# Kernel optimization log

Hardware: AMD Instinct MI355X
Metric: run time of the kernel (lower is better)

Reference implementation:

```python
import jax, jax.numpy as jnp
import numpy as np

B, N, D, H, C, TOPK = 1, 1024, 1024, 16, 64, 2
HD = D // H   # head_dim = 64
G = N // C    # num blocks = 16


def setup_inputs() -> dict:
    key = jax.random.key(0)
    ks = jax.random.split(key, 6)
    s = 0.02  # init_std
    x = jax.random.normal(ks[0], (B, N, D), jnp.float32)
    Wq = jax.random.normal(ks[1], (D, D), jnp.float32) * s
    Wk = jax.random.normal(ks[2], (D, D), jnp.float32) * s
    Wv = jax.random.normal(ks[3], (D, D), jnp.float32) * s
    Wg = jax.random.normal(ks[4], (2 * H, D), jnp.float32) * s
    Wo = jax.random.normal(ks[5], (D, D), jnp.float32) * s
    return {"x": x, "Wq": Wq, "Wk": Wk, "Wv": Wv, "Wg": Wg, "Wo": Wo}


def reference(x, Wq, Wk, Wv, Wg, Wo):
    b, n, d = x.shape
    h, c, hd, g = H, C, HD, G
    scale = hd ** -0.5
    # projections (torch Linear: x @ W.T)
    q = (x @ Wq.T).reshape(b, n, h, hd)
    k = (x @ Wk.T).reshape(b, n, h, hd)
    v = (x @ Wv.T).reshape(b, n, h, hd)
    gate = jax.nn.softmax((x @ Wg.T).reshape(b, n, h, 2), axis=-1)
    # chunked views: (b, g, c, h, hd)
    kc = k.reshape(b, g, c, h, hd)
    vc = v.reshape(b, g, c, h, hd)
    # compressed block keys: mean over chunk dim -> (b, g, h, hd)
    k_compress = kc.mean(axis=2)
    # block selection scores (b, h, n, g)
    score = jnp.einsum('bnhd,bghd->bhng', q, k_compress)
    pos = jnp.arange(n)[:, None]
    blk = jnp.arange(g)[None, :]
    mask = pos >= c * blk  # (n, g), exactly as source's _get_mask (masked_fill where True)
    score = jnp.where(mask[None, None], -jnp.inf, score)
    idx = jax.lax.top_k(score, TOPK)[1]  # (b, h, n, top_k), int indices
    # gather selected blocks per (batch, head, query)
    k_bhgcd = kc.transpose(0, 3, 1, 2, 4)  # (b, h, g, c, hd)
    v_bhgcd = vc.transpose(0, 3, 1, 2, 4)
    gather = jax.vmap(jax.vmap(lambda kv, i: kv[i]))  # over b, h
    k_sel = gather(k_bhgcd, idx).reshape(b, h, n, TOPK * c, hd)
    v_sel = gather(v_bhgcd, idx).reshape(b, h, n, TOPK * c, hd)
    # inter: per-query attention over gathered KV (non-causal), flash-attn scale 1/sqrt(hd)
    logits = jnp.einsum('bnhd,bhnld->bhnl', q, k_sel) * scale
    p = jax.nn.softmax(logits, axis=-1)
    o_inter = jnp.einsum('bhnl,bhnld->bnhd', p, v_sel)
    # intra: causal attention within each chunk
    qc = q.reshape(b, g, c, h, hd)
    intra = jnp.einsum('bgihd,bgjhd->bghij', qc, kc) * scale
    cm = jnp.tril(jnp.ones((c, c), dtype=bool))
    intra = jnp.where(cm, intra, -jnp.inf)
    pi = jax.nn.softmax(intra, axis=-1)
    o_intra = jnp.einsum('bghij,bgjhd->bgihd', pi, vc).reshape(b, n, h, hd)
    # gated blend + output projection
    o = gate[..., 0:1] * o_inter + gate[..., 1:2] * o_intra  # (b, n, h, hd)
    return o.reshape(b, n, h * hd) @ Wo.T
```

## Files before the change

kernel.cpp:

```cpp
#include <hip/hip_runtime.h>
#include <hip/hip_bf16.h>
#include <math.h>


typedef __attribute__((ext_vector_type(8))) short short8;
typedef __attribute__((ext_vector_type(4))) float f32x4;

#define NTOK 1024
#define DMODEL 1024
#define NHEAD 16
#define HDIM 64
#define CHUNK 64
#define NBLK 16

__device__ __forceinline__ float qmax16(float v)
{
    #pragma unroll
    for (int off = 1; off < 16; off <<= 1) v = fmaxf(v, __shfl_xor(v, off));
    return v;
}

__device__ __forceinline__ float qsum16(float v)
{
    #pragma unroll
    for (int off = 1; off < 16; off <<= 1) v += __shfl_xor(v, off);
    return v;
}

__global__ __launch_bounds__(256) void prep_kernel(
    const float* __restrict__ x,  const float* __restrict__ Wq,
    const float* __restrict__ Wk, const float* __restrict__ Wv,
    const float* __restrict__ Wo, const float* __restrict__ Wg,
    __hip_bfloat16* __restrict__ xh,  __hip_bfloat16* __restrict__ xl,
    __hip_bfloat16* __restrict__ Wqh,
    __hip_bfloat16* __restrict__ Wkh, __hip_bfloat16* __restrict__ Wvh,
    __hip_bfloat16* __restrict__ Woh, __hip_bfloat16* __restrict__ Wol,
    float* __restrict__ xm, float2* __restrict__ gate)
{
    __shared__ float gs[32];
    const int bid = blockIdx.x;
    if (bid < 5120) {
        const int which = bid >> 10;
        const int b = bid & 1023;
        const int i = (b * 256 + threadIdx.x) * 4;
        const float* in; __hip_bfloat16 *hi, *lo = nullptr;
        if (which == 0)      { in = x;  hi = xh;  lo = xl; }
        else if (which == 1) { in = Wq; hi = Wqh; }
        else if (which == 2) { in = Wk; hi = Wkh; }
        else if (which == 3) { in = Wv; hi = Wvh; }
        else                 { in = Wo; hi = Woh; lo = Wol; }
        float4 v = *(const float4*)(in + i);
        float vv[4] = {v.x, v.y, v.z, v.w};
        __hip_bfloat16 h[4], l[4];
        #pragma unroll
        for (int j = 0; j < 4; j++) {
            h[j] = __float2bfloat16(vv[j]);
            l[j] = __float2bfloat16(vv[j] - __bfloat162float(h[j]));
        }
        *(uint2*)(hi + i) = *(uint2*)h;
        if (lo) *(uint2*)(lo + i) = *(uint2*)l;
    } else if (bid < 5184) {
        const int b = bid - 5120;
        const int g = b >> 2;
        const int f = (b & 3) * 256 + threadIdx.x;
        float s = 0.f;
        #pragma unroll 8
        for (int c = 0; c < CHUNK; c++) s += x[(size_t)(g * CHUNK + c) * DMODEL + f];
        xm[g * DMODEL + f] = s * (1.0f / CHUNK);
    } else {
        const int n = bid - 5184;
        const int wave = threadIdx.x >> 6, lane = threadIdx.x & 63;
        #pragma unroll
        for (int jj = 0; jj < 8; jj++) {
            int j = wave * 8 + jj;
            float s = 0.f;
            #pragma unroll
            for (int t = 0; t < 16; t++) {
                int d = lane + (t << 6);
                s += x[n * DMODEL + d] * Wg[j * DMODEL + d];
            }
            #pragma unroll
            for (int off = 32; off; off >>= 1) s += __shfl_xor(s, off);
            if (lane == 0) gs[j] = s;
        }
        __syncthreads();
        if (threadIdx.x < NHEAD) {
            int h = threadIdx.x;
            float a = gs[2 * h], b = gs[2 * h + 1];
            float m = fmaxf(a, b);
            float ea = expf(a - m), eb = expf(b - m);
            float inv = 1.f / (ea + eb);
            gate[n * NHEAD + h] = make_float2(ea * inv, eb * inv);
        }
    }
}

__global__ __launch_bounds__(256) void kc_gemm_kernel(
    const float* __restrict__ xm, const float* __restrict__ Wk,
    float* __restrict__ kc)
{
    const int f = blockIdx.x;
    const int g = threadIdx.x >> 4;
    const int sub = threadIdx.x & 15;
    const float* wrow = Wk + (size_t)f * DMODEL;
    float s = 0.f;
    #pragma unroll 16
    for (int i = 0; i < 64; i++) {
        int e = i * 16 + sub;
        s += xm[g * DMODEL + e] * wrow[e];
    }
    #pragma unroll
    for (int off = 8; off; off >>= 1) s += __shfl_xor(s, off);
    if (sub == 0) kc[g * DMODEL + f] = s;
}

__global__ __launch_bounds__(256) void u_kernel(
    const float* __restrict__ kc, const float* __restrict__ Wq,
    __hip_bfloat16* __restrict__ Uh, __hip_bfloat16* __restrict__ Ul)
{
    __shared__ float kcs[64];
    const int h = blockIdx.x >> 4, g = blockIdx.x & 15;
    if (threadIdx.x < 64) kcs[threadIdx.x] = kc[g * DMODEL + h * HDIM + threadIdx.x];
    __syncthreads();
    const int col = (h << 4) | g;
    for (int f = threadIdx.x; f < DMODEL; f += 256) {
        float s = 0.f;
        #pragma unroll 16
        for (int d = 0; d < 64; d++)
            s += kcs[d] * Wq[(size_t)(h * HDIM + d) * DMODEL + f];
        __hip_bfloat16 hv = __float2bfloat16(s);
        Uh[(size_t)col * DMODEL + f] = hv;
        Ul[(size_t)col * DMODEL + f] = __float2bfloat16(s - __bfloat162float(hv));
    }
}

__global__ __launch_bounds__(256) void qkv_score_kernel(
    const __hip_bfloat16* __restrict__ xh, const __hip_bfloat16* __restrict__ xl,
    const __hip_bfloat16* __restrict__ Wqh, const __hip_bfloat16* __restrict__ Wkh,
    const __hip_bfloat16* __restrict__ Wvh,
    const __hip_bfloat16* __restrict__ Uh, const __hip_bfloat16* __restrict__ Ul,
    __hip_bfloat16* __restrict__ Qb, __hip_bfloat16* __restrict__ Kb,
    __hip_bfloat16* __restrict__ Vt, float* __restrict__ S)
{
    __shared__ uint4 smem4[36864 / 16];
    char* smem = (char*)smem4;
    const int b = blockIdx.x;

    const int tid  = threadIdx.x;
    const int wave = tid >> 6;
    const int lane = tid & 63;
    const int lr = tid >> 2;
    const int lc = (tid & 3) * 16;
    const int wm = (wave >> 1) * 32;
    const int wn = (wave & 1) * 32;
    const int fr = lane & 15;
    const int quad = lane >> 4;

    if (b < 768) {
        __hip_bfloat16 (*Ash)[72] = (__hip_bfloat16(*)[72])smem;
        __hip_bfloat16 (*Bsh)[72] = (__hip_bfloat16(*)[72])(smem + 9216);

        const int widx = b >> 8;
        const int t = b & 255;
        const __hip_bfloat16* __restrict__ Bh =
            (widx == 0) ? Wqh : (widx == 1) ? Wkh : Wvh;
        const int n0 = (t & 15) * 64;
        const int m0 = (t >> 4) * 64;

        f32x4 acc[2][2] = {};

        for (int k0 = 0; k0 < DMODEL; k0 += 64) {
            const size_t aoff = (size_t)(m0 + lr) * DMODEL + k0 + lc;
            const size_t boff = (size_t)(n0 + lr) * DMODEL + k0 + lc;
            *(uint4*)(&Ash[lr][lc])     = *(const uint4*)(xh + aoff);
            *(uint4*)(&Ash[lr][lc + 8]) = *(const uint4*)(xh + aoff + 8);
            *(uint4*)(&Bsh[lr][lc])     = *(const uint4*)(Bh + boff);
            *(uint4*)(&Bsh[lr][lc + 8]) = *(const uint4*)(Bh + boff + 8);
            __syncthreads();

            #pragma unroll
            for (int hk = 0; hk < 2; hk++) {
                const int kc0 = hk * 32 + quad * 8;
                short8 a0 = *(const short8*)(&Ash[wm + fr][kc0]);
                short8 a1 = *(const short8*)(&Ash[wm + 16 + fr][kc0]);
                short8 b0 = *(const short8*)(&Bsh[wn + fr][kc0]);
                short8 b1 = *(const short8*)(&Bsh[wn + 16 + fr][kc0]);
                acc[0][0] = __builtin_amdgcn_mfma_f32_16x16x32_bf16(a0, b0, acc[0][0], 0, 0, 0);
                acc[0][1] = __builtin_amdgcn_mfma_f32_16x16x32_bf16(a0, b1, acc[0][1], 0, 0, 0);
                acc[1][0] = __builtin_amdgcn_mfma_f32_16x16x32_bf16(a1, b0, acc[1][0], 0, 0, 0);
                acc[1][1] = __builtin_amdgcn_mfma_f32_16x16x32_bf16(a1, b1, acc[1][1], 0, 0, 0);
            }
            __syncthreads();
        }

        if (widx == 0) {
            #pragma unroll
            for (int tm = 0; tm < 2; tm++)
            #pragma unroll
            for (int tn = 0; tn < 2; tn++)
            #pragma unroll
            for (int r = 0; r < 4; r++) {
                int row = m0 + wm + tm * 16 + quad * 4 + r;
                int col = n0 + wn + tn * 16 + fr;
                Qb[(size_t)row * DMODEL + col] = __float2bfloat16(acc[tm][tn][r]);
            }
        } else if (widx == 1) {
            #pragma unroll
            for (int tm = 0; tm < 2; tm++)
            #pragma unroll
            for (int tn = 0; tn < 2; tn++)
            #pragma unroll
            for (int r = 0; r < 4; r++) {
                int row = m0 + wm + tm * 16 + quad * 4 + r;
                int col = n0 + wn + tn * 16 + fr;
                Kb[(size_t)row * DMODEL + col] = __float2bfloat16(acc[tm][tn][r]);
            }
        } else {
            __hip_bfloat16 (*T)[72] = (__hip_bfloat16(*)[72])smem;
            #pragma unroll
            for (int tm = 0; tm < 2; tm++)
            #pragma unroll
            for (int tn = 0; tn < 2; tn++)
            #pragma unroll
            for (int r = 0; r < 4; r++) {
                int nloc = wm + tm * 16 + quad * 4 + r;
                int floc = wn + tn * 16 + fr;
                T[floc][nloc] = __float2bfloat16(acc[tm][tn][r]);
            }
            __syncthreads();
            const size_t o = (size_t)(n0 + lr) * NTOK + m0 + lc;
            *(uint4*)(Vt + o)     = *(uint4*)(&T[lr][lc]);
            *(uint4*)(Vt + o + 8) = *(uint4*)(&T[lr][lc + 8]);
        }
    } else {
        __hip_bfloat16 (*Ash)[72] = (__hip_bfloat16(*)[72])smem;
        __hip_bfloat16 (*Asl)[72] = (__hip_bfloat16(*)[72])(smem + 9216);
        __hip_bfloat16 (*Bsh)[72] = (__hip_bfloat16(*)[72])(smem + 18432);
        __hip_bfloat16 (*Bsl)[72] = (__hip_bfloat16(*)[72])(smem + 27648);

        const int bb = b - 768;
        const int m0 = (bb >> 2) * 64;
        const int n0 = (bb & 3) * 64;

        f32x4 acc[2][2] = {};

        for (int k0 = 0; k0 < DMODEL; k0 += 64) {
            const size_t aoff = (size_t)(m0 + lr) * DMODEL + k0 + lc;
            const size_t boff = (size_t)(n0 + lr) * DMODEL + k0 + lc;
            *(uint4*)(&Ash[lr][lc])     = *(const uint4*)(xh + aoff);
            *(uint4*)(&Ash[lr][lc + 8]) = *(const uint4*)(xh + aoff + 8);
            *(uint4*)(&Asl[lr][lc])     = *(const uint4*)(xl + aoff);
            *(uint4*)(&Asl[lr][lc + 8]) = *(const uint4*)(xl + aoff + 8);
            *(uint4*)(&Bsh[lr][lc])     = *(const uint4*)(Uh + boff);
            *(uint4*)(&Bsh[lr][lc + 8]) = *(const uint4*)(Uh + boff + 8);
            *(uint4*)(&Bsl[lr][lc])     = *(const uint4*)(Ul + boff);
            *(uint4*)(&Bsl[lr][lc + 8]) = *(const uint4*)(Ul + boff + 8);
            __syncthreads();

            #pragma unroll
            for (int hk = 0; hk < 2; hk++) {
                const int kc0 = hk * 32 + quad * 8;
                short8 a0h = *(const short8*)(&Ash[wm + fr][kc0]);
                short8 a1h = *(const short8*)(&Ash[wm + 16 + fr][kc0]);
                short8 a0l = *(const short8*)(&Asl[wm + fr][kc0]);
                short8 a1l = *(const short8*)(&Asl[wm + 16 + fr][kc0]);
                short8 b0h = *(const short8*)(&Bsh[wn + fr][kc0]);
                short8 b1h = *(const short8*)(&Bsh[wn + 16 + fr][kc0]);
                short8 b0l = *(const short8*)(&Bsl[wn + fr][kc0]);
                short8 b1l = *(const short8*)(&Bsl[wn + 16 + fr][kc0]);
                acc[0][0] = __builtin_amdgcn_mfma_f32_16x16x32_bf16(a0l, b0h, acc[0][0], 0, 0, 0);
                acc[0][1] = __builtin_amdgcn_mfma_f32_16x16x32_bf16(a0l, b1h, acc[0][1], 0, 0, 0);
                acc[1][0] = __builtin_amdgcn_mfma_f32_16x16x32_bf16(a1l, b0h, acc[1][0], 0, 0, 0);
                acc[1][1] = __builtin_amdgcn_mfma_f32_16x16x32_bf16(a1l, b1h, acc[1][1], 0, 0, 0);
                acc[0][0] = __builtin_amdgcn_mfma_f32_16x16x32_bf16(a0h, b0l, acc[0][0], 0, 0, 0);
                acc[0][1] = __builtin_amdgcn_mfma_f32_16x16x32_bf16(a0h, b1l, acc[0][1], 0, 0, 0);
                acc[1][0] = __builtin_amdgcn_mfma_f32_16x16x32_bf16(a1h, b0l, acc[1][0], 0, 0, 0);
                acc[1][1] = __builtin_amdgcn_mfma_f32_16x16x32_bf16(a1h, b1l, acc[1][1], 0, 0, 0);
                acc[0][0] = __builtin_amdgcn_mfma_f32_16x16x32_bf16(a0h, b0h, acc[0][0], 0, 0, 0);
                acc[0][1] = __builtin_amdgcn_mfma_f32_16x16x32_bf16(a0h, b1h, acc[0][1], 0, 0, 0);
                acc[1][0] = __builtin_amdgcn_mfma_f32_16x16x32_bf16(a1h, b0h, acc[1][0], 0, 0, 0);
                acc[1][1] = __builtin_amdgcn_mfma_f32_16x16x32_bf16(a1h, b1h, acc[1][1], 0, 0, 0);
            }
            __syncthreads();
        }

        #pragma unroll
        for (int tm = 0; tm < 2; tm++)
        #pragma unroll
        for (int tn = 0; tn < 2; tn++)
        #pragma unroll
        for (int r = 0; r < 4; r++) {
            int row = m0 + wm + tm * 16 + quad * 4 + r;
            int col = n0 + wn + tn * 16 + fr;
            S[(size_t)row * 256 + col] = acc[tm][tn][r];
        }
    }
}

__global__ __launch_bounds__(256, 4) void attn_mfma_kernel(
    const __hip_bfloat16* __restrict__ Qb, const __hip_bfloat16* __restrict__ Kb,
    const __hip_bfloat16* __restrict__ Vt, const float* __restrict__ S,
    const float2* __restrict__ gate, __hip_bfloat16* __restrict__ oh)
{
    __shared__ float OS[4][16][64];
    __shared__ float OIs[16][64];
    __shared__ float mS[4][16], lS[4][16], liS[16];
    __shared__ int i1s[16], i2s[16];
    __shared__ float2 sgate[16];
    __shared__ unsigned unionMask;
    __shared__ __hip_bfloat16 Ps[4][16][72];

    const int bid = blockIdx.x;
    const int qt = bid & 3;
    const int h  = (bid >> 2) & 15;
    const int g  = bid >> 6;
    const int tid = threadIdx.x;
    const int s = tid >> 6;
    const int lane = tid & 63;
    const int fr = lane & 15, quad = lane >> 4;

    if (tid < 16) {
        const int n = g * 64 + qt * 16 + tid;
        const float* Sn = S + (size_t)n * 256 + h * 16;
        float sc[NBLK];
        #pragma unroll
        for (int gg = 0; gg < NBLK; gg++)
            sc[gg] = (n >= (gg << 6)) ? -INFINITY : Sn[gg];
        int i1 = -1, i2 = -1;
        float b1 = -INFINITY;
        #pragma unroll
        for (int gg = 0; gg < NBLK; gg++) if (i1 < 0 || sc[gg] > b1) { b1 = sc[gg]; i1 = gg; }
        float b2 = -INFINITY;
        #pragma unroll
        for (int gg = 0; gg < NBLK; gg++) { if (gg == i1) continue; if (i2 < 0 || sc[gg] > b2) { b2 = sc[gg]; i2 = gg; } }
        i1s[tid] = i1; i2s[tid] = i2;
        sgate[tid] = gate[(size_t)n * NHEAD + h];
        unsigned m = (1u << i1) | (1u << i2);
        #pragma unroll
        for (int off = 1; off < 16; off <<= 1) m |= (unsigned)__shfl_xor((int)m, off);
        if (tid == 0) unionMask = m;
    }
    __syncthreads();

    const unsigned um = unionMask;

    const size_t qrow = (size_t)(g * 64 + qt * 16 + fr) * DMODEL + h * HDIM + quad * 8;
    const short8 qa0 = *(const short8*)(Qb + qrow);
    const short8 qa1 = *(const short8*)(Qb + qrow + 32);

    int qi1[4], qi2[4];
    #pragma unroll
    for (int r = 0; r < 4; r++) {
        int q = quad * 4 + r;
        qi1[r] = i1s[q]; qi2[r] = i2s[q];
    }

    f32x4 Oint[4] = {};
    float mrun[4] = {-INFINITY, -INFINITY, -INFINITY, -INFINITY};
    float lrun[4] = {0.f, 0.f, 0.f, 0.f};

    const __hip_bfloat16* __restrict__ Kh = Kb + h * HDIM + quad * 8;
    const __hip_bfloat16* __restrict__ Vh = Vt + (size_t)(h * HDIM) * NTOK + quad * 8;

    int j = 0;
    for (int kb = 0; kb < NBLK; kb++) {
        if (!((um >> kb) & 1u)) continue;
        if ((j++ & 3) != s) continue;

        f32x4 sacc[4] = {};
        #pragma unroll
        for (int t = 0; t < 4; t++) {
            const size_t krow = (size_t)(kb * 64 + t * 16 + fr) * DMODEL;
            short8 kb0 = *(const short8*)(Kh + krow);
            short8 kb1 = *(const short8*)(Kh + krow + 32);
            sacc[t] = __builtin_amdgcn_mfma_f32_16x16x32_bf16(qa0, kb0, sacc[t], 0, 0, 0);
            sacc[t] = __builtin_amdgcn_mfma_f32_16x16x32_bf16(qa1, kb1, sacc[t], 0, 0, 0);
        }

        #pragma unroll
        for (int r = 0; r < 4; r++) {
            const bool sel = (kb == qi1[r]) | (kb == qi2[r]);
            float v0 = sacc[0][r] * 0.125f, v1 = sacc[1][r] * 0.125f;
            float v2 = sacc[2][r] * 0.125f, v3 = sacc[3][r] * 0.125f;
            float mx = qmax16(fmaxf(fmaxf(v0, v1), fmaxf(v2, v3)));
            float mnew = sel ? fmaxf(mrun[r], mx) : mrun[r];
            float f = sel ? __expf(mrun[r] - mnew) : 1.0f;
            float e0 = sel ? __expf(v0 - mnew) : 0.f;
            float e1 = sel ? __expf(v1 - mnew) : 0.f;
            float e2 = sel ? __expf(v2 - mnew) : 0.f;
            float e3 = sel ? __expf(v3 - mnew) : 0.f;
            float es = qsum16(e0 + e1 + e2 + e3);
            lrun[r] = lrun[r] * f + es;
            mrun[r] = mnew;
            #pragma unroll
            for (int dn = 0; dn < 4; dn++) Oint[dn][r] *= f;
            const int prow = quad * 4 + r;
            Ps[s][prow][ 0 + fr] = __float2bfloat16(e0);
            Ps[s][prow][16 + fr] = __float2bfloat16(e1);
            Ps[s][prow][32 + fr] = __float2bfloat16(e2);
            Ps[s][prow][48 + fr] = __float2bfloat16(e3);
        }

        short8 pa0 = *(const short8*)(&Ps[s][fr][quad * 8]);
        short8 pa1 = *(const short8*)(&Ps[s][fr][32 + quad * 8]);
        #pragma unroll
        for (int dn = 0; dn < 4; dn++) {
            const size_t vrow = (size_t)(dn * 16 + fr) * NTOK + kb * 64;
            short8 v0 = *(const short8*)(Vh + vrow);
            short8 v1 = *(const short8*)(Vh + vrow + 32);
            Oint[dn] = __builtin_amdgcn_mfma_f32_16x16x32_bf16(pa0, v0, Oint[dn], 0, 0, 0);
            Oint[dn] = __builtin_amdgcn_mfma_f32_16x16x32_bf16(pa1, v1, Oint[dn], 0, 0, 0);
        }
    }

    if ((j & 3) == s) {
        f32x4 sacc[4] = {};
        #pragma unroll
        for (int t = 0; t < 4; t++) {
            const size_t krow = (size_t)(g * 64 + t * 16 + fr) * DMODEL;
            short8 kb0 = *(const short8*)(Kh + krow);
            short8 kb1 = *(const short8*)(Kh + krow + 32);
            sacc[t] = __builtin_amdgcn_mfma_f32_16x16x32_bf16(qa0, kb0, sacc[t], 0, 0, 0);
            sacc[t] = __builtin_amdgcn_mfma_f32_16x16x32_bf16(qa1, kb1, sacc[t], 0, 0, 0);
        }
        f32x4 Ointr[4] = {};
        #pragma unroll
        for (int r = 0; r < 4; r++) {
            const int qloc = qt * 16 + quad * 4 + r;
            float vv[4];
            #pragma unroll
            for (int t = 0; t < 4; t++) {
                const int col = t * 16 + fr;
                float v = sacc[t][r] * 0.125f;
                vv[t] = (col <= qloc) ? v : -INFINITY;
            }
            float mx = qmax16(fmaxf(fmaxf(vv[0], vv[1]), fmaxf(vv[2], vv[3])));
            float e0 = __expf(vv[0] - mx), e1 = __expf(vv[1] - mx);
            float e2 = __expf(vv[2] - mx), e3 = __expf(vv[3] - mx);
            float lsum = qsum16(e0 + e1 + e2 + e3);
            const int prow = quad * 4 + r;
            if (fr == 0) liS[prow] = lsum;
            Ps[s][prow][ 0 + fr] = __float2bfloat16(e0);
            Ps[s][prow][16 + fr] = __float2bfloat16(e1);
            Ps[s][prow][32 + fr] = __float2bfloat16(e2);
            Ps[s][prow][48 + fr] = __float2bfloat16(e3);
        }
        short8 pa0 = *(const short8*)(&Ps[s][fr][quad * 8]);
        short8 pa1 = *(const short8*)(&Ps[s][fr][32 + quad * 8]);
        #pragma unroll
        for (int dn = 0; dn < 4; dn++) {
            const size_t vrow = (size_t)(dn * 16 + fr) * NTOK + g * 64;
            short8 v0 = *(const short8*)(Vh + vrow);
            short8 v1 = *(const short8*)(Vh + vrow + 32);
            Ointr[dn] = __builtin_amdgcn_mfma_f32_16x16x32_bf16(pa0, v0, Ointr[dn], 0, 0, 0);
            Ointr[dn] = __builtin_amdgcn_mfma_f32_16x16x32_bf16(pa1, v1, Ointr[dn], 0, 0, 0);
        }
        #pragma unroll
        for (int r = 0; r < 4; r++)
        #pragma unroll
        for (int dn = 0; dn < 4; dn++)
            OIs[quad * 4 + r][dn * 16 + fr] = Ointr[dn][r];
    }

    #pragma unroll
    for (int r = 0; r < 4; r++) {
        if (fr == 0) { mS[s][quad * 4 + r] = mrun[r]; lS[s][quad * 4 + r] = lrun[r]; }
        #pragma unroll
        for (int dn = 0; dn < 4; dn++)
            OS[s][quad * 4 + r][dn * 16 + fr] = Oint[dn][r];
    }
    __syncthreads();

    {
        const int q = tid >> 4;
        const int db = (tid & 15) * 4;
        float M = fmaxf(fmaxf(mS[0][q], mS[1][q]), fmaxf(mS[2][q], mS[3][q]));
        float L = 0.f;
        float o0 = 0.f, o1 = 0.f, o2 = 0.f, o3 = 0.f;
        #pragma unroll
        for (int ss = 0; ss < 4; ss++) {
            float p = __expf(mS[ss][q] - M);
            L += lS[ss][q] * p;
            o0 += OS[ss][q][db + 0] * p;
            o1 += OS[ss][q][db + 1] * p;
            o2 += OS[ss][q][db + 2] * p;
            o3 += OS[ss][q][db + 3] * p;
        }
        const float2 gt = sgate[q];
        const float wi = gt.x / L;
        const float wl = gt.y / liS[q];
        unsigned short out4[4];
        out4[0] = __builtin_bit_cast(unsigned short, __float2bfloat16(wi * o0 + wl * OIs[q][db + 0]));
        out4[1] = __builtin_bit_cast(unsigned short, __float2bfloat16(wi * o1 + wl * OIs[q][db + 1]));
        out4[2] = __builtin_bit_cast(unsigned short, __float2bfloat16(wi * o2 + wl * OIs[q][db + 2]));
        out4[3] = __builtin_bit_cast(unsigned short, __float2bfloat16(wi * o3 + wl * OIs[q][db + 3]));
        const int n = g * 64 + qt * 16 + q;
        *(uint2*)(oh + (size_t)n * DMODEL + h * HDIM + db) = *(uint2*)out4;
    }
}

__global__ __launch_bounds__(256) void gemm_wo(
    const __hip_bfloat16* __restrict__ Ah,
    const __hip_bfloat16* __restrict__ Bh, const __hip_bfloat16* __restrict__ Bl,
    float* __restrict__ C)
{
    __shared__ alignas(16) __hip_bfloat16 Ash[64][72];
    __shared__ alignas(16) __hip_bfloat16 Bsh[64][72];
    __shared__ alignas(16) __hip_bfloat16 Bsl[64][72];

    const int n0 = blockIdx.x * 64;
    const int m0 = blockIdx.y * 64;

    const int tid  = threadIdx.x;
    const int wave = tid >> 6;
    const int lane = tid & 63;
    const int lr = tid >> 2;
    const int lc = (tid & 3) * 16;
    const int wm = (wave >> 1) * 32;
    const int wn = (wave & 1) * 32;
    const int fr = lane & 15;
    const int quad = lane >> 4;

    f32x4 acc[2][2] = {};

    for (int k0 = 0; k0 < DMODEL; k0 += 64) {
        const size_t aoff = (size_t)(m0 + lr) * DMODEL + k0 + lc;
        const size_t boff = (size_t)(n0 + lr) * DMODEL + k0 + lc;
        *(uint4*)(&Ash[lr][lc])     = *(const uint4*)(Ah + aoff);
        *(uint4*)(&Ash[lr][lc + 8]) = *(const uint4*)(Ah + aoff + 8);
        *(uint4*)(&Bsh[lr][lc])     = *(const uint4*)(Bh + boff);
        *(uint4*)(&Bsh[lr][lc + 8]) = *(const uint4*)(Bh + boff + 8);
        *(uint4*)(&Bsl[lr][lc])     = *(const uint4*)(Bl + boff);
        *(uint4*)(&Bsl[lr][lc + 8]) = *(const uint4*)(Bl + boff + 8);
        __syncthreads();

        #pragma unroll
        for (int hk = 0; hk < 2; hk++) {
            const int kc0 = hk * 32 + quad * 8;
            short8 a0 = *(const short8*)(&Ash[wm + fr][kc0]);
            short8 a1 = *(const short8*)(&Ash[wm + 16 + fr][kc0]);
            short8 b0h = *(const short8*)(&Bsh[wn + fr][kc0]);
            short8 b1h = *(const short8*)(&Bsh[wn + 16 + fr][kc0]);
            short8 b0l = *(const short8*)(&Bsl[wn + fr][kc0]);
            short8 b1l = *(const short8*)(&Bsl[wn + 16 + fr][kc0]);
            acc[0][0] = __builtin_amdgcn_mfma_f32_16x16x32_bf16(a0, b0l, acc[0][0], 0, 0, 0);
            acc[0][1] = __builtin_amdgcn_mfma_f32_16x16x32_bf16(a0, b1l, acc[0][1], 0, 0, 0);
            acc[1][0] = __builtin_amdgcn_mfma_f32_16x16x32_bf16(a1, b0l, acc[1][0], 0, 0, 0);
            acc[1][1] = __builtin_amdgcn_mfma_f32_16x16x32_bf16(a1, b1l, acc[1][1], 0, 0, 0);
            acc[0][0] = __builtin_amdgcn_mfma_f32_16x16x32_bf16(a0, b0h, acc[0][0], 0, 0, 0);
            acc[0][1] = __builtin_amdgcn_mfma_f32_16x16x32_bf16(a0, b1h, acc[0][1], 0, 0, 0);
            acc[1][0] = __builtin_amdgcn_mfma_f32_16x16x32_bf16(a1, b0h, acc[1][0], 0, 0, 0);
            acc[1][1] = __builtin_amdgcn_mfma_f32_16x16x32_bf16(a1, b1h, acc[1][1], 0, 0, 0);
        }
        __syncthreads();
    }

    #pragma unroll
    for (int tm = 0; tm < 2; tm++)
    #pragma unroll
    for (int tn = 0; tn < 2; tn++)
    #pragma unroll
    for (int r = 0; r < 4; r++) {
        int row = m0 + wm + tm * 16 + quad * 4 + r;
        int col = n0 + wn + tn * 16 + fr;
        C[(size_t)row * DMODEL + col] = acc[tm][tn][r];
    }
}

extern "C" void kernel_launch(void* const* d_in, const int* in_sizes, int n_in,
                              void* d_out, int out_size, void* d_ws, size_t ws_size,
                              hipStream_t stream)
{
    const float* x  = (const float*)d_in[0];
    const float* Wq = (const float*)d_in[1];
    const float* Wk = (const float*)d_in[2];
    const float* Wv = (const float*)d_in[3];
    const float* Wg = (const float*)d_in[4];
    const float* Wo = (const float*)d_in[5];

    const size_t M1 = (size_t)NTOK * DMODEL;

    float* S       = (float*)d_ws;
    float* xm      = S + (size_t)NTOK * 256;
    float* kc      = xm + NBLK * DMODEL;
    float2* gate   = (float2*)(kc + NBLK * DMODEL);
    __hip_bfloat16* xh  = (__hip_bfloat16*)(gate + NTOK * NHEAD);
    __hip_bfloat16* xl  = xh + M1;
    __hip_bfloat16* Wqh = xl + M1;
    __hip_bfloat16* Wkh = Wqh + M1;
    __hip_bfloat16* Wvh = Wkh + M1;
    __hip_bfloat16* Woh = Wvh + M1;
    __hip_bfloat16* Wol = Woh + M1;
    __hip_bfloat16* oh  = Wol + M1;
    __hip_bfloat16* Uh  = oh + M1;
    __hip_bfloat16* Ul  = Uh + 256 * DMODEL;
    __hip_bfloat16* Qb  = Ul + 256 * DMODEL;
    __hip_bfloat16* Kb  = Qb + M1;
    __hip_bfloat16* Vt  = Kb + M1;

    prep_kernel<<<6208, 256, 0, stream>>>(
        x, Wq, Wk, Wv, Wo, Wg, xh, xl, Wqh, Wkh, Wvh, Woh, Wol, xm, gate);

    kc_gemm_kernel<<<1024, 256, 0, stream>>>(xm, Wk, kc);
    u_kernel<<<256, 256, 0, stream>>>(kc, Wq, Uh, Ul);

    qkv_score_kernel<<<832, 256, 0, stream>>>(
        xh, xl, Wqh, Wkh, Wvh, Uh, Ul, Qb, Kb, Vt, S);

    attn_mfma_kernel<<<NBLK * NHEAD * 4, 256, 0, stream>>>(Qb, Kb, Vt, S, gate, oh);

    dim3 gwo(16, 16);
    gemm_wo<<<gwo, 256, 0, stream>>>(oh, Woh, Wol, (float*)d_out);
}
```

Measured before the change: 178.8 us.

## Stage GEMM tiles with direct global-to-LDS loads and XOR-swizzled layout

Replaces register-staged global loads into padded LDS tiles with global_load_lds 16-byte direct-to-LDS transfers into an XOR-swizzled unpadded layout in qkv_score and gemm_wo. gemm_wo moves to 512 threads with 8 waves each computing a 16x32 subtile, which doubles the waves per block. The attention intra path also accumulates into a separate register array. The aim is to cut VGPR traffic and LDS bank conflicts on tile staging, at the cost of relying on a swizzle whose correctness must match the fragment reads.

```diff
diff --git a/kernel.cpp b/kernel.cpp
--- a/kernel.cpp
+++ b/kernel.cpp
@@ -25,6 +25,37 @@
     #pragma unroll
     for (int off = 1; off < 16; off <<= 1) v += __shfl_xor(v, off);
     return v;
+}
+
+
+#define GLOAD_LDS16(gp, lp)                                              \
+    __builtin_amdgcn_global_load_lds(                                    \
+        (const __attribute__((address_space(1))) void*)(gp),             \
+        (__attribute__((address_space(3))) void*)(lp), 16, 0, 0)
+
+__device__ __forceinline__ void stage64(const __hip_bfloat16* __restrict__ g0,
+                                        __hip_bfloat16* t, int wave, int lane)
+{
+    const int sub = lane >> 3;
+    const int cch = (lane & 7) ^ sub;
+    #pragma unroll
+    for (int j = 0; j < 2; j++) {
+        const int rr = (2 * wave + j) * 8 + sub;
+        GLOAD_LDS16(g0 + (size_t)rr * DMODEL + cch * 8, t + (2 * wave + j) * 512);
+    }
+}
+
+__device__ __forceinline__ void stage64w8(const __hip_bfloat16* __restrict__ g0,
+                                          __hip_bfloat16* t, int wave, int lane)
+{
+    const int sub = lane >> 3;
+    const int cch = (lane & 7) ^ sub;
+    GLOAD_LDS16(g0 + (size_t)(wave * 8 + sub) * DMODEL + cch * 8, t + wave * 512);
+}
+
+__device__ __forceinline__ short8 ldsfrag(const __hip_bfloat16* t, int row, int chunk)
+{
+    return *(const short8*)((const char*)t + row * 128 + (((chunk) ^ (row & 7)) << 4));
 }
 
 __global__ __launch_bounds__(256) void prep_kernel(
@@ -142,10 +173,13 @@
     __hip_bfloat16* __restrict__ Qb, __hip_bfloat16* __restrict__ Kb,
     __hip_bfloat16* __restrict__ Vt, float* __restrict__ S)
 {
-    __shared__ uint4 smem4[36864 / 16];
-    char* smem = (char*)smem4;
+    __shared__ alignas(16) char smem[32768];
+    __hip_bfloat16* AshP = (__hip_bfloat16*)smem;
+    __hip_bfloat16* AslP = (__hip_bfloat16*)(smem + 8192);
+    __hip_bfloat16* BshP = (__hip_bfloat16*)(smem + 16384);
+    __hip_bfloat16* BslP = (__hip_bfloat16*)(smem + 24576);
+
     const int b = blockIdx.x;
-
     const int tid  = threadIdx.x;
     const int wave = tid >> 6;
     const int lane = tid & 63;
@@ -157,9 +191,6 @@
     const int quad = lane >> 4;
 
     if (b < 768) {
-        __hip_bfloat16 (*Ash)[72] = (__hip_bfloat16(*)[72])smem;
-        __hip_bfloat16 (*Bsh)[72] = (__hip_bfloat16(*)[72])(smem + 9216);
-
         const int widx = b >> 8;
         const int t = b & 255;
         const __hip_bfloat16* __restrict__ Bh =
@@ -170,21 +201,17 @@
         f32x4 acc[2][2] = {};
 
         for (int k0 = 0; k0 < DMODEL; k0 += 64) {
-            const size_t aoff = (size_t)(m0 + lr) * DMODEL + k0 + lc;
-            const size_t boff = (size_t)(n0 + lr) * DMODEL + k0 + lc;
-            *(uint4*)(&Ash[lr][lc])     = *(const uint4*)(xh + aoff);
-            *(uint4*)(&Ash[lr][lc + 8]) = *(const uint4*)(xh + aoff + 8);
-            *(uint4*)(&Bsh[lr][lc])     = *(const uint4*)(Bh + boff);
-            *(uint4*)(&Bsh[lr][lc + 8]) = *(const uint4*)(Bh + boff + 8);
+            stage64(xh + (size_t)m0 * DMODEL + k0, AshP, wave, lane);
+            stage64(Bh + (size_t)n0 * DMODEL + k0, BshP, wave, lane);
             __syncthreads();
 
             #pragma unroll
             for (int hk = 0; hk < 2; hk++) {
-                const int kc0 = hk * 32 + quad * 8;
-                short8 a0 = *(const short8*)(&Ash[wm + fr][kc0]);
-                short8 a1 = *(const short8*)(&Ash[wm + 16 + fr][kc0]);
-                short8 b0 = *(const short8*)(&Bsh[wn + fr][kc0]);
-                short8 b1 = *(const short8*)(&Bsh[wn + 16 + fr][kc0]);
+                const int ch = hk * 4 + quad;
+                short8 a0 = ldsfrag(AshP, wm + fr, ch);
+                short8 a1 = ldsfrag(AshP, wm + 16 + fr, ch);
+                short8 b0 = ldsfrag(BshP, wn + fr, ch);
+                short8 b1 = ldsfrag(BshP, wn + 16 + fr, ch);
                 acc[0][0] = __builtin_amdgcn_mfma_f32_16x16x32_bf16(a0, b0, acc[0][0], 0, 0, 0);
                 acc[0][1] = __builtin_amdgcn_mfma_f32_16x16x32_bf16(a0, b1, acc[0][1], 0, 0, 0);
                 acc[1][0] = __builtin_amdgcn_mfma_f32_16x16x32_bf16(a1, b0, acc[1][0], 0, 0, 0);
@@ -233,11 +260,6 @@
             *(uint4*)(Vt + o + 8) = *(uint4*)(&T[lr][lc + 8]);
         }
     } else {
-        __hip_bfloat16 (*Ash)[72] = (__hip_bfloat16(*)[72])smem;
-        __hip_bfloat16 (*Asl)[72] = (__hip_bfloat16(*)[72])(smem + 9216);
-        __hip_bfloat16 (*Bsh)[72] = (__hip_bfloat16(*)[72])(smem + 18432);
-        __hip_bfloat16 (*Bsl)[72] = (__hip_bfloat16(*)[72])(smem + 27648);
-
         const int bb = b - 768;
         const int m0 = (bb >> 2) * 64;
         const int n0 = (bb & 3) * 64;
@@ -245,29 +267,23 @@
         f32x4 acc[2][2] = {};
 
         for (int k0 = 0; k0 < DMODEL; k0 += 64) {
-            const size_t aoff = (size_t)(m0 + lr) * DMODEL + k0 + lc;
-            const size_t boff = (size_t)(n0 + lr) * DMODEL + k0 + lc;
-            *(uint4*)(&Ash[lr][lc])     = *(const uint4*)(xh + aoff);
-            *(uint4*)(&Ash[lr][lc + 8]) = *(const uint4*)(xh + aoff + 8);
-            *(uint4*)(&Asl[lr][lc])     = *(const uint4*)(xl + aoff);
-            *(uint4*)(&Asl[lr][lc + 8]) = *(const uint4*)(xl + aoff + 8);
-            *(uint4*)(&Bsh[lr][lc])     = *(const uint4*)(Uh + boff);
-            *(uint4*)(&Bsh[lr][lc + 8]) = *(const uint4*)(Uh + boff + 8);
-            *(uint4*)(&Bsl[lr][lc])     = *(const uint4*)(Ul + boff);
-            *(uint4*)(&Bsl[lr][lc + 8]) = *(const uint4*)(Ul + boff + 8);
+            stage64(xh + (size_t)m0 * DMODEL + k0, AshP, wave, lane);
+            stage64(xl + (size_t)m0 * DMODEL + k0, AslP, wave, lane);
+            stage64(Uh + (size_t)n0 * DMODEL + k0, BshP, wave, lane);
+            stage64(Ul + (size_t)n0 * DMODEL + k0, BslP, wave, lane);
             __syncthreads();
 
             #pragma unroll
             for (int hk = 0; hk < 2; hk++) {
-                const int kc0 = hk * 32 + quad * 8;
-                short8 a0h = *(const short8*)(&Ash[wm + fr][kc0]);
-                short8 a1h = *(const short8*)(&Ash[wm + 16 + fr][kc0]);
-                short8 a0l = *(const short8*)(&Asl[wm + fr][kc0]);
-                short8 a1l = *(const short8*)(&Asl[wm + 16 + fr][kc0]);
-                short8 b0h = *(const short8*)(&Bsh[wn + fr][kc0]);
-                short8 b1h = *(const short8*)(&Bsh[wn + 16 + fr][kc0]);
-                short8 b0l = *(const short8*)(&Bsl[wn + fr][kc0]);
-                short8 b1l = *(const short8*)(&Bsl[wn + 16 + fr][kc0]);
+                const int ch = hk * 4 + quad;
+                short8 a0h = ldsfrag(AshP, wm + fr, ch);
+                short8 a1h = ldsfrag(AshP, wm + 16 + fr, ch);
+                short8 a0l = ldsfrag(AslP, wm + fr, ch);
+                short8 a1l = ldsfrag(AslP, wm + 16 + fr, ch);
+                short8 b0h = ldsfrag(BshP, wn + fr, ch);
+                short8 b1h = ldsfrag(BshP, wn + 16 + fr, ch);
+                short8 b0l = ldsfrag(BslP, wn + fr, ch);
+                short8 b1l = ldsfrag(BslP, wn + 16 + fr, ch);
                 acc[0][0] = __builtin_amdgcn_mfma_f32_16x16x32_bf16(a0l, b0h, acc[0][0], 0, 0, 0);
                 acc[0][1] = __builtin_amdgcn_mfma_f32_16x16x32_bf16(a0l, b1h, acc[0][1], 0, 0, 0);
                 acc[1][0] = __builtin_amdgcn_mfma_f32_16x16x32_bf16(a1l, b0h, acc[1][0], 0, 0, 0);
@@ -447,19 +463,20 @@
         }
         short8 pa0 = *(const short8*)(&Ps[s][fr][quad * 8]);
         short8 pa1 = *(const short8*)(&Ps[s][fr][32 + quad * 8]);
+        f32x4 Ointr2[4] = {};
         #pragma unroll
         for (int dn = 0; dn < 4; dn++) {
             const size_t vrow = (size_t)(dn * 16 + fr) * NTOK + g * 64;
             short8 v0 = *(const short8*)(Vh + vrow);
             short8 v1 = *(const short8*)(Vh + vrow + 32);
-            Ointr[dn] = __builtin_amdgcn_mfma_f32_16x16x32_bf16(pa0, v0, Ointr[dn], 0, 0, 0);
-            Ointr[dn] = __builtin_amdgcn_mfma_f32_16x16x32_bf16(pa1, v1, Ointr[dn], 0, 0, 0);
+            Ointr2[dn] = __builtin_amdgcn_mfma_f32_16x16x32_bf16(pa0, v0, Ointr[dn], 0, 0, 0);
+            Ointr2[dn] = __builtin_amdgcn_mfma_f32_16x16x32_bf16(pa1, v1, Ointr2[dn], 0, 0, 0);
         }
         #pragma unroll
         for (int r = 0; r < 4; r++)
         #pragma unroll
         for (int dn = 0; dn < 4; dn++)
-            OIs[quad * 4 + r][dn * 16 + fr] = Ointr[dn][r];
+            OIs[quad * 4 + r][dn * 16 + fr] = Ointr2[dn][r];
     }
 
     #pragma unroll
@@ -499,14 +516,15 @@
     }
 }
 
-__global__ __launch_bounds__(256) void gemm_wo(
+__global__ __launch_bounds__(512) void gemm_wo(
     const __hip_bfloat16* __restrict__ Ah,
     const __hip_bfloat16* __restrict__ Bh, const __hip_bfloat16* __restrict__ Bl,
     float* __restrict__ C)
 {
-    __shared__ alignas(16) __hip_bfloat16 Ash[64][72];
-    __shared__ alignas(16) __hip_bfloat16 Bsh[64][72];
-    __shared__ alignas(16) __hip_bfloat16 Bsl[64][72];
+    __shared__ alignas(16) char smem[24576];
+    __hip_bfloat16* AshP = (__hip_bfloat16*)smem;
+    __hip_bfloat16* BshP = (__hip_bfloat16*)(smem + 8192);
+    __hip_bfloat16* BslP = (__hip_bfloat16*)(smem + 16384);
 
     const int n0 = blockIdx.x * 64;
     const int m0 = blockIdx.y * 64;
@@ -514,56 +532,42 @@
     const int tid  = threadIdx.x;
     const int wave = tid >> 6;
     const int lane = tid & 63;
-    const int lr = tid >> 2;
-    const int lc = (tid & 3) * 16;
-    const int wm = (wave >> 1) * 32;
+    const int wm = (wave >> 1) * 16;
     const int wn = (wave & 1) * 32;
     const int fr = lane & 15;
     const int quad = lane >> 4;
 
-    f32x4 acc[2][2] = {};
+    f32x4 acc[2] = {};
 
     for (int k0 = 0; k0 < DMODEL; k0 += 64) {
-        const size_t aoff = (size_t)(m0 + lr) * DMODEL + k0 + lc;
-        const size_t boff = (size_t)(n0 + lr) * DMODEL + k0 + lc;
-        *(uint4*)(&Ash[lr][lc])     = *(const uint4*)(Ah + aoff);
-        *(uint4*)(&Ash[lr][lc + 8]) = *(const uint4*)(Ah + aoff + 8);
-        *(uint4*)(&Bsh[lr][lc])     = *(const uint4*)(Bh + boff);
-        *(uint4*)(&Bsh[lr][lc + 8]) = *(const uint4*)(Bh + boff + 8);
-        *(uint4*)(&Bsl[lr][lc])     = *(const uint4*)(Bl + boff);
-        *(uint4*)(&Bsl[lr][lc + 8]) = *(const uint4*)(Bl + boff + 8);
+        stage64w8(Ah + (size_t)m0 * DMODEL + k0, AshP, wave, lane);
+        stage64w8(Bh + (size_t)n0 * DMODEL + k0, BshP, wave, lane);
+        stage64w8(Bl + (size_t)n0 * DMODEL + k0, BslP, wave, lane);
         __syncthreads();
 
         #pragma unroll
         for (int hk = 0; hk < 2; hk++) {
-            const int kc0 = hk * 32 + quad * 8;
-            short8 a0 = *(const short8*)(&Ash[wm + fr][kc0]);
-            short8 a1 = *(const short8*)(&Ash[wm + 16 + fr][kc0]);
-            short8 b0h = *(const short8*)(&Bsh[wn + fr][kc0]);
-            short8 b1h = *(const short8*)(&Bsh[wn + 16 + fr][kc0]);
-            short8 b0l = *(const short8*)(&Bsl[wn + fr][kc0]);
-            short8 b1l = *(const short8*)(&Bsl[wn + 16 + fr][kc0]);
-            acc[0][0] = __builtin_amdgcn_mfma_f32_16x16x32_bf16(a0, b0l, acc[0][0], 0, 0, 0);
-            acc[0][1] = __builtin_amdgcn_mfma_f32_16x16x32_bf16(a0, b1l, acc[0][1], 0, 0, 0);
-            acc[1][0] = __builtin_amdgcn_mfma_f32_16x16x32_bf16(a1, b0l, acc[1][0], 0, 0, 0);
-            acc[1][1] = __builtin_amdgcn_mfma_f32_16x16x32_bf16(a1, b1l, acc[1][1], 0, 0, 0);
-            acc[0][0] = __builtin_amdgcn_mfma_f32_16x16x32_bf16(a0, b0h, acc[0][0], 0, 0, 0);
-            acc[0][1] = __builtin_amdgcn_mfma_f32_16x16x32_bf16(a0, b1h, acc[0][1], 0, 0, 0);
-            acc[1][0] = __builtin_amdgcn_mfma_f32_16x16x32_bf16(a1, b0h, acc[1][0], 0, 0, 0);
-            acc[1][1] = __builtin_amdgcn_mfma_f32_16x16x32_bf16(a1, b1h, acc[1][1], 0, 0, 0);
+            const int ch = hk * 4 + quad;
+            short8 a0  = ldsfrag(AshP, wm + fr, ch);
+            short8 b0h = ldsfrag(BshP, wn + fr, ch);
+            short8 b1h = ldsfrag(BshP, wn + 16 + fr, ch);
+            short8 b0l = ldsfrag(BslP, wn + fr, ch);
+            short8 b1l = ldsfrag(BslP, wn + 16 + fr, ch);
+            acc[0] = __builtin_amdgcn_mfma_f32_16x16x32_bf16(a0, b0l, acc[0], 0, 0, 0);
+            acc[1] = __builtin_amdgcn_mfma_f32_16x16x32_bf16(a0, b1l, acc[1], 0, 0, 0);
+            acc[0] = __builtin_amdgcn_mfma_f32_16x16x32_bf16(a0, b0h, acc[0], 0, 0, 0);
+            acc[1] = __builtin_amdgcn_mfma_f32_16x16x32_bf16(a0, b1h, acc[1], 0, 0, 0);
         }
         __syncthreads();
     }
 
     #pragma unroll
-    for (int tm = 0; tm < 2; tm++)
-    #pragma unroll
     for (int tn = 0; tn < 2; tn++)
     #pragma unroll
     for (int r = 0; r < 4; r++) {
-        int row = m0 + wm + tm * 16 + quad * 4 + r;
+        int row = m0 + wm + quad * 4 + r;
         int col = n0 + wn + tn * 16 + fr;
-        C[(size_t)row * DMODEL + col] = acc[tm][tn][r];
+        C[(size_t)row * DMODEL + col] = acc[tn][r];
     }
 }
 
@@ -610,5 +614,5 @@
     attn_mfma_kernel<<<NBLK * NHEAD * 4, 256, 0, stream>>>(Qb, Kb, Vt, S, gate, oh);
 
     dim3 gwo(16, 16);
-    gemm_wo<<<gwo, 256, 0, stream>>>(oh, Woh, Wol, (float*)d_out);
-}
+    gemm_wo<<<gwo, 512, 0, stream>>>(oh, Woh, Wol, (float*)d_out);
+}
```

New measurement: 161.8 us. 1.1x faster.
